# Optimization experiments

Measured on AMD Instinct MI355X. Metric: run time of the kernel, lower is better.

Reference implementation:

```python
import jax, jax.numpy as jnp
import numpy as np

B, C, H, W = 8, 64, 64, 64


def setup_inputs() -> dict:
    key = jax.random.key(0)
    ks = jax.random.split(key, 8)
    s = 1.0 / np.sqrt(C)  # keep logits in a reasonable range
    return {
        "x": jax.random.normal(ks[0], (B, C, H, W), dtype=jnp.float32),
        "Wf": jax.random.normal(ks[1], (C, C), dtype=jnp.float32) * s,
        "bf": jax.random.normal(ks[2], (C,), dtype=jnp.float32) * s,
        "Wg": jax.random.normal(ks[3], (C, C), dtype=jnp.float32) * s,
        "bg": jax.random.normal(ks[4], (C,), dtype=jnp.float32) * s,
        "Wh": jax.random.normal(ks[5], (C, C), dtype=jnp.float32) * s,
        "bh": jax.random.normal(ks[6], (C,), dtype=jnp.float32) * s,
        "gamma": jax.random.normal(ks[7], (1,), dtype=jnp.float32),
    }


def reference(x, Wf, bf, Wg, bg, Wh, bh, gamma):
    b, c, h, w = x.shape
    n = h * w
    xf = x.reshape(b, c, n)  # [B, C, N]
    # 1x1 convs == per-pixel channel GEMMs
    f = jnp.einsum("oc,bcn->bon", Wf, xf) + bf[None, :, None]  # [B, C, N]
    g = jnp.einsum("oc,bcn->bon", Wg, xf) + bg[None, :, None]
    hh = jnp.einsum("oc,bcn->bon", Wh, xf) + bh[None, :, None]
    # att_in[b, i, j] = f[b, :, i] . g[b, :, j]  (f_x permuted then bmm with g_x)
    att = jax.nn.softmax(jnp.einsum("bci,bcj->bij", f, g), axis=-1)  # [B, N, N]
    # torch.bmm(h_x, attention): out[b, c, j] = sum_i h[b, c, i] * att[b, i, j]
    out = jnp.einsum("bci,bij->bcj", hh, att).reshape(b, c, h, w)
    return gamma[0] * out + x
```

## Files before the change

### kernel.cpp

```cpp
#include <hip/hip_runtime.h>

#define BB 8
#define CC 64
#define NN 4096
#define ICH 4
#define JCH 8
#define LOG2E 1.4426950408889634f

typedef float f32x4  __attribute__((ext_vector_type(4)));
typedef float f32x16 __attribute__((ext_vector_type(16)));
typedef _Float16 half8_t __attribute__((ext_vector_type(8)));
typedef _Float16 half4_t __attribute__((ext_vector_type(4)));


__global__ __launch_bounds__(64) void qkv_kernel(
    const float* __restrict__ x,
    const float* __restrict__ Wf, const float* __restrict__ bf,
    const float* __restrict__ Wg, const float* __restrict__ bg,
    const float* __restrict__ Wh, const float* __restrict__ bh,
    _Float16* __restrict__ fT, _Float16* __restrict__ gT,
    _Float16* __restrict__ hT)
{
    const int split = blockIdx.x;
    const int z     = split >> 2;
    const int o0    = (split & 3) * 16;
    const int n     = blockIdx.y * 64 + threadIdx.x;
    const int b     = blockIdx.z;
    const float* W    = (z == 0) ? Wf : ((z == 1) ? Wg : Wh);
    const float* bias = (z == 0) ? bf : ((z == 1) ? bg : bh);

    float xv[CC];
    const float* xp = x + (size_t)b * CC * NN + n;
#pragma unroll
    for (int c = 0; c < CC; ++c) xv[c] = xp[(size_t)c * NN];

    if (z < 2) {
        _Float16* dst = ((z == 0) ? fT : gT) + (size_t)(b * NN + n) * CC + o0;
        const float scale = (z == 0) ? LOG2E : 1.0f;
#pragma unroll
        for (int o8 = 0; o8 < 2; ++o8) {
            half8_t v;
#pragma unroll
            for (int oo = 0; oo < 8; ++oo) {
                const int o = o0 + o8 * 8 + oo;
                float acc = bias[o];
#pragma unroll
                for (int c = 0; c < CC; ++c) acc += W[o * CC + c] * xv[c];
                v[oo] = (_Float16)(acc * scale);
            }
            *(half8_t*)(dst + o8 * 8) = v;
        }
    } else {
        _Float16* hdst = hT + ((size_t)(b * (NN / 32) + (n >> 5)) * CC) * 32 + (n & 31);
#pragma unroll
        for (int o = o0; o < o0 + 16; ++o) {
            float acc = bias[o];
#pragma unroll
            for (int c = 0; c < CC; ++c) acc += W[o * CC + c] * xv[c];
            hdst[o * 32] = (_Float16)acc;
        }
    }
}

__global__ __launch_bounds__(256, 4) void stats_kernel(
    const _Float16* __restrict__ fT, const _Float16* __restrict__ gT,
    float* __restrict__ lpart)
{
    __shared__ _Float16 gbuf[2][64][72];

    const int lane = threadIdx.x & 63;
    const int wv   = threadIdx.x >> 6;
    const int b    = blockIdx.y;
    const int jc   = blockIdx.z;
    const int i0   = blockIdx.x * 128 + wv * 32;
    const int l31  = lane & 31;
    const int q5   = lane >> 5;

    half8_t a[4];
    const _Float16* fa = fT + (size_t)(b * NN + i0 + l31) * CC + q5 * 8;
#pragma unroll
    for (int kc = 0; kc < 4; ++kc) a[kc] = *(const half8_t*)(fa + kc * 16);

    const _Float16* gchunk = gT + (size_t)(b * NN + jc * (NN / JCH)) * CC;
    const int T = NN / JCH / 64;

    const int srow = wv * 16 + (lane >> 3);
    const int scol = (lane & 7) * 8;

    {
        const half8_t v0 = *(const half8_t*)(gchunk + (size_t)srow * CC + scol);
        const half8_t v1 = *(const half8_t*)(gchunk + (size_t)(srow + 8) * CC + scol);
        *(half8_t*)&gbuf[0][srow][scol] = v0;
        *(half8_t*)&gbuf[0][srow + 8][scol] = v1;
    }
    __syncthreads();

    float l16[16];
#pragma unroll
    for (int r = 0; r < 16; ++r) l16[r] = 0.f;

    for (int t = 0; t < T; ++t) {
        const int buf = t & 1;
        const bool pf = (t + 1 < T);
        half8_t p0, p1;
        if (pf) {
            const _Float16* src = gchunk + (size_t)((t + 1) * 64 + srow) * CC + scol;
            p0 = *(const half8_t*)(src);
            p1 = *(const half8_t*)(src + 8 * CC);
        }
#pragma unroll
        for (int js = 0; js < 2; ++js) {
            const _Float16* grow = &gbuf[buf][js * 32 + l31][0] + q5 * 8;
            f32x16 s = {};
#pragma unroll
            for (int kc = 0; kc < 4; ++kc) {
                const half8_t bfr = *(const half8_t*)(grow + kc * 16);
                s = __builtin_amdgcn_mfma_f32_32x32x16_f16(a[kc], bfr, s, 0, 0, 0);
            }
#pragma unroll
            for (int r = 0; r < 16; ++r) l16[r] += __builtin_exp2f(s[r]);
        }
        if (pf) {
            *(half8_t*)&gbuf[buf ^ 1][srow][scol] = p0;
            *(half8_t*)&gbuf[buf ^ 1][srow + 8][scol] = p1;
        }
        __syncthreads();
    }

#pragma unroll
    for (int r = 0; r < 16; ++r) {
#pragma unroll
        for (int off = 1; off < 32; off <<= 1)
            l16[r] += __shfl_xor(l16[r], off);
    }

    if (l31 == 0) {
        float* lp = lpart + (size_t)jc * BB * NN + b * NN + i0;
#pragma unroll
        for (int rb = 0; rb < 4; ++rb) {
            f32x4 v;
#pragma unroll
            for (int k = 0; k < 4; ++k) v[k] = l16[rb * 4 + k];
            *(f32x4*)(lp + rb * 8 + q5 * 4) = v;
        }
    }
}

__global__ __launch_bounds__(256) void rmerge_kernel(
    const float* __restrict__ lpart, float* __restrict__ nbias)
{
    const int idx = blockIdx.x * 256 + threadIdx.x;
    float s = 0.f;
#pragma unroll
    for (int jc = 0; jc < JCH; ++jc) s += lpart[(size_t)jc * BB * NN + idx];
    nbias[idx] = -__builtin_log2f(s);
}

__global__ __launch_bounds__(256, 4) void attn_kernel(
    const _Float16* __restrict__ fT, const _Float16* __restrict__ gT,
    const _Float16* __restrict__ hT, const float* __restrict__ nbias,
    _Float16* __restrict__ pout)
{
    __shared__ _Float16 fbuf[2][32][72];
    __shared__ _Float16 hbuf[2][64][40];
    __shared__ _Float16 Pbuf[4][32][40];

    const int lane = threadIdx.x & 63;
    const int wv   = threadIdx.x >> 6;
    const int b    = blockIdx.y;
    const int ic   = blockIdx.z;
    const int l31  = lane & 31;
    const int q5   = lane >> 5;
    const int j0   = blockIdx.x * 128 + wv * 32;
    const int j    = j0 + l31;

    half8_t bg[4];
    const _Float16* grow = gT + (size_t)(b * NN + j) * CC + q5 * 8;
#pragma unroll
    for (int kc = 0; kc < 4; ++kc) bg[kc] = *(const half8_t*)(grow + kc * 16);

    f32x16 acc[2] = {};

    const int ibase = ic * (NN / ICH);
    const _Float16* fchunk = fT + ((size_t)b * NN + ibase) * CC;
    const _Float16* htile0 = hT + ((size_t)(b * (NN / 32) + ibase / 32) * CC) * 32;
    const float*    nb     = nbias + b * NN + ibase;
    const int T = (NN / ICH) / 32;

    const int tid    = threadIdx.x;
    const int frow_s = tid >> 3;
    const int fcol_s = (tid & 7) * 8;
    const int hoff_s = tid * 8;
    const int hrow_s = tid >> 2;
    const int hcol_s = (tid & 3) * 8;

    {
        const half8_t fv = *(const half8_t*)(fchunk + (size_t)frow_s * CC + fcol_s);
        const half8_t hv = *(const half8_t*)(htile0 + hoff_s);
        *(half8_t*)&fbuf[0][frow_s][fcol_s] = fv;
        *(half8_t*)&hbuf[0][hrow_s][hcol_s] = hv;
    }
    __syncthreads();

    for (int t = 0; t < T; ++t) {
        const int buf = t & 1;
        const bool pf = (t + 1 < T);
        half8_t pfv, phv;
        if (pf) {
            pfv = *(const half8_t*)(fchunk + (size_t)((t + 1) * 32 + frow_s) * CC + fcol_s);
            phv = *(const half8_t*)(htile0 + (size_t)(t + 1) * CC * 32 + hoff_s);
        }

        f32x16 s;
        {
#pragma unroll
            for (int rb = 0; rb < 4; ++rb) {
                const f32x4 n4 = *(const f32x4*)(nb + t * 32 + rb * 8 + q5 * 4);
#pragma unroll
                for (int k = 0; k < 4; ++k) s[rb * 4 + k] = n4[k];
            }
        }
        const _Float16* frow = &fbuf[buf][l31][0] + q5 * 8;
#pragma unroll
        for (int kc = 0; kc < 4; ++kc) {
            const half8_t af = *(const half8_t*)(frow + kc * 16);
            s = __builtin_amdgcn_mfma_f32_32x32x16_f16(af, bg[kc], s, 0, 0, 0);
        }
#pragma unroll
        for (int rb = 0; rb < 4; ++rb) {
            half4_t pv;
#pragma unroll
            for (int k = 0; k < 4; ++k)
                pv[k] = (_Float16)__builtin_exp2f(s[rb * 4 + k]);
            *(half4_t*)&Pbuf[wv][l31][rb * 8 + q5 * 4] = pv;
        }
        __builtin_amdgcn_wave_barrier();

#pragma unroll
        for (int kk = 0; kk < 2; ++kk) {
            const half8_t pb = *(const half8_t*)(&Pbuf[wv][l31][0] + kk * 16 + q5 * 8);
#pragma unroll
            for (int ct = 0; ct < 2; ++ct) {
                const half8_t ah = *(const half8_t*)(&hbuf[buf][ct * 32 + l31][0] + kk * 16 + q5 * 8);
                acc[ct] = __builtin_amdgcn_mfma_f32_32x32x16_f16(ah, pb, acc[ct], 0, 0, 0);
            }
        }
        if (pf) {
            *(half8_t*)&fbuf[buf ^ 1][frow_s][fcol_s] = pfv;
            *(half8_t*)&hbuf[buf ^ 1][hrow_s][hcol_s] = phv;
        }
        __syncthreads();
    }

    _Float16* pb_out = pout + (((size_t)ic * BB + b) * CC) * NN;
#pragma unroll
    for (int ct = 0; ct < 2; ++ct) {
#pragma unroll
        for (int r = 0; r < 16; ++r) {
            const int c = ct * 32 + (r & 3) + 8 * (r >> 2) + 4 * q5;
            pb_out[(size_t)c * NN + j] = (_Float16)acc[ct][r];
        }
    }
}

__global__ __launch_bounds__(256) void combine_kernel(
    const float* __restrict__ x, const float* __restrict__ gammap,
    const _Float16* __restrict__ pout, float* __restrict__ out)
{
    const float gam = gammap[0];
    const size_t i8 = ((size_t)blockIdx.x * 256 + threadIdx.x) * 8;
    const size_t TOT = (size_t)BB * CC * NN;

    float s[8] = {0.f, 0.f, 0.f, 0.f, 0.f, 0.f, 0.f, 0.f};
#pragma unroll
    for (int ic = 0; ic < ICH; ++ic) {
        const half8_t p = *(const half8_t*)(pout + ic * TOT + i8);
#pragma unroll
        for (int k = 0; k < 8; ++k) s[k] += (float)p[k];
    }
    const f32x4 x0 = *(const f32x4*)(x + i8);
    const f32x4 x1 = *(const f32x4*)(x + i8 + 4);
    f32x4 o0, o1;
#pragma unroll
    for (int k = 0; k < 4; ++k) { o0[k] = gam * s[k] + x0[k]; o1[k] = gam * s[k + 4] + x1[k]; }
    *(f32x4*)(out + i8) = o0;
    *(f32x4*)(out + i8 + 4) = o1;
}

extern "C" void kernel_launch(void* const* d_in, const int* in_sizes, int n_in,
                              void* d_out, int out_size, void* d_ws, size_t ws_size,
                              hipStream_t stream) {
    const float* x     = (const float*)d_in[0];
    const float* Wf    = (const float*)d_in[1];
    const float* bf    = (const float*)d_in[2];
    const float* Wg    = (const float*)d_in[3];
    const float* bg    = (const float*)d_in[4];
    const float* Wh    = (const float*)d_in[5];
    const float* bh    = (const float*)d_in[6];
    const float* gamma = (const float*)d_in[7];
    float* out = (float*)d_out;

    const size_t TOT = (size_t)BB * CC * NN;
    _Float16* fT   = (_Float16*)d_ws;
    _Float16* gT   = fT + TOT;
    _Float16* hT   = gT + TOT;
    _Float16* pout = hT + TOT;
    float* lpart   = (float*)(pout + (size_t)ICH * TOT);
    float* nbias   = lpart + (size_t)JCH * BB * NN;

    qkv_kernel<<<dim3(12, NN / 64, BB), 64, 0, stream>>>(
        x, Wf, bf, Wg, bg, Wh, bh, fT, gT, hT);
    stats_kernel<<<dim3(NN / 128, BB, JCH), 256, 0, stream>>>(fT, gT, lpart);
    rmerge_kernel<<<dim3(BB * NN / 256), 256, 0, stream>>>(lpart, nbias);
    attn_kernel<<<dim3(NN / 128, BB, ICH), 256, 0, stream>>>(fT, gT, hT, nbias, pout);
    combine_kernel<<<dim3(TOT / (256 * 8)), 256, 0, stream>>>(x, gamma, pout, out);
}
```

Before: 191.9 us.

## Keep softmax probabilities in registers via cross-lane shuffle and double i-split

The attention kernel no longer writes exp'd scores to a shared-memory P buffer and reads them back as the MFMA B operand. It rearranges the accumulator layout into operand layout with lane-xor-32 shuffles, which removes LDS traffic and a wave barrier per tile. It also doubles the number of i-chunks from 4 to 8 when the workspace is large enough, giving more blocks for occupancy. The cost is twice the partial-output traffic in the combine kernel.

```diff
diff --git a/kernel.cpp b/kernel.cpp
--- a/kernel.cpp
+++ b/kernel.cpp
@@ -3,7 +3,6 @@
 #define BB 8
 #define CC 64
 #define NN 4096
-#define ICH 4
 #define JCH 8
 #define LOG2E 1.4426950408889634f
 
@@ -11,6 +10,9 @@
 typedef float f32x16 __attribute__((ext_vector_type(16)));
 typedef _Float16 half8_t __attribute__((ext_vector_type(8)));
 typedef _Float16 half4_t __attribute__((ext_vector_type(4)));
+typedef _Float16 half2_t __attribute__((ext_vector_type(2)));
+
+typedef union { half8_t v8; half2_t v2[4]; } h8u;
 
 
 __global__ __launch_bounds__(64) void qkv_kernel(
@@ -163,16 +165,15 @@
 {
     __shared__ _Float16 fbuf[2][32][72];
     __shared__ _Float16 hbuf[2][64][40];
-    __shared__ _Float16 Pbuf[4][32][40];
 
     const int lane = threadIdx.x & 63;
     const int wv   = threadIdx.x >> 6;
     const int b    = blockIdx.y;
     const int ic   = blockIdx.z;
+    const int nic  = gridDim.z;
     const int l31  = lane & 31;
     const int q5   = lane >> 5;
-    const int j0   = blockIdx.x * 128 + wv * 32;
-    const int j    = j0 + l31;
+    const int j    = blockIdx.x * 128 + wv * 32 + l31;
 
     half8_t bg[4];
     const _Float16* grow = gT + (size_t)(b * NN + j) * CC + q5 * 8;
@@ -181,11 +182,12 @@
 
     f32x16 acc[2] = {};
 
-    const int ibase = ic * (NN / ICH);
+    const int ichunk = NN / nic;
+    const int ibase  = ic * ichunk;
     const _Float16* fchunk = fT + ((size_t)b * NN + ibase) * CC;
     const _Float16* htile0 = hT + ((size_t)(b * (NN / 32) + ibase / 32) * CC) * 32;
     const float*    nb     = nbias + b * NN + ibase;
-    const int T = (NN / ICH) / 32;
+    const int T = ichunk / 32;
 
     const int tid    = threadIdx.x;
     const int frow_s = tid >> 3;
@@ -226,25 +228,46 @@
             const half8_t af = *(const half8_t*)(frow + kc * 16);
             s = __builtin_amdgcn_mfma_f32_32x32x16_f16(af, bg[kc], s, 0, 0, 0);
         }
-#pragma unroll
-        for (int rb = 0; rb < 4; ++rb) {
-            half4_t pv;
-#pragma unroll
-            for (int k = 0; k < 4; ++k)
-                pv[k] = (_Float16)__builtin_exp2f(s[rb * 4 + k]);
-            *(half4_t*)&Pbuf[wv][l31][rb * 8 + q5 * 4] = pv;
-        }
-        __builtin_amdgcn_wave_barrier();
-
-#pragma unroll
-        for (int kk = 0; kk < 2; ++kk) {
-            const half8_t pb = *(const half8_t*)(&Pbuf[wv][l31][0] + kk * 16 + q5 * 8);
-#pragma unroll
-            for (int ct = 0; ct < 2; ++ct) {
-                const half8_t ah = *(const half8_t*)(&hbuf[buf][ct * 32 + l31][0] + kk * 16 + q5 * 8);
-                acc[ct] = __builtin_amdgcn_mfma_f32_32x32x16_f16(ah, pb, acc[ct], 0, 0, 0);
-            }
-        }
+
+        half2_t P[8];
+#pragma unroll
+        for (int r8 = 0; r8 < 8; ++r8) {
+            half2_t v;
+            v[0] = (_Float16)__builtin_exp2f(s[r8 * 2]);
+            v[1] = (_Float16)__builtin_exp2f(s[r8 * 2 + 1]);
+            P[r8] = v;
+        }
+
+        const int sA = __builtin_bit_cast(int, q5 ? P[0] : P[2]);
+        const int sB = __builtin_bit_cast(int, q5 ? P[1] : P[3]);
+        const int sC = __builtin_bit_cast(int, q5 ? P[4] : P[6]);
+        const int sD = __builtin_bit_cast(int, q5 ? P[5] : P[7]);
+        const half2_t rA = __builtin_bit_cast(half2_t, __shfl_xor(sA, 32, 64));
+        const half2_t rB = __builtin_bit_cast(half2_t, __shfl_xor(sB, 32, 64));
+        const half2_t rC = __builtin_bit_cast(half2_t, __shfl_xor(sC, 32, 64));
+        const half2_t rD = __builtin_bit_cast(half2_t, __shfl_xor(sD, 32, 64));
+
+        h8u B0, B1;
+        B0.v2[0] = q5 ? rA   : P[0];
+        B0.v2[1] = q5 ? rB   : P[1];
+        B0.v2[2] = q5 ? P[2] : rA;
+        B0.v2[3] = q5 ? P[3] : rB;
+        B1.v2[0] = q5 ? rC   : P[4];
+        B1.v2[1] = q5 ? rD   : P[5];
+        B1.v2[2] = q5 ? P[6] : rC;
+        B1.v2[3] = q5 ? P[7] : rD;
+
+#pragma unroll
+        for (int ct = 0; ct < 2; ++ct) {
+            const half8_t ah0 = *(const half8_t*)(&hbuf[buf][ct * 32 + l31][0] + q5 * 8);
+            acc[ct] = __builtin_amdgcn_mfma_f32_32x32x16_f16(ah0, B0.v8, acc[ct], 0, 0, 0);
+        }
+#pragma unroll
+        for (int ct = 0; ct < 2; ++ct) {
+            const half8_t ah1 = *(const half8_t*)(&hbuf[buf][ct * 32 + l31][0] + 16 + q5 * 8);
+            acc[ct] = __builtin_amdgcn_mfma_f32_32x32x16_f16(ah1, B1.v8, acc[ct], 0, 0, 0);
+        }
+
         if (pf) {
             *(half8_t*)&fbuf[buf ^ 1][frow_s][fcol_s] = pfv;
             *(half8_t*)&hbuf[buf ^ 1][hrow_s][hcol_s] = phv;
@@ -265,15 +288,14 @@
 
 __global__ __launch_bounds__(256) void combine_kernel(
     const float* __restrict__ x, const float* __restrict__ gammap,
-    const _Float16* __restrict__ pout, float* __restrict__ out)
+    const _Float16* __restrict__ pout, float* __restrict__ out, int nic)
 {
     const float gam = gammap[0];
     const size_t i8 = ((size_t)blockIdx.x * 256 + threadIdx.x) * 8;
     const size_t TOT = (size_t)BB * CC * NN;
 
     float s[8] = {0.f, 0.f, 0.f, 0.f, 0.f, 0.f, 0.f, 0.f};
-#pragma unroll
-    for (int ic = 0; ic < ICH; ++ic) {
+    for (int ic = 0; ic < nic; ++ic) {
         const half8_t p = *(const half8_t*)(pout + ic * TOT + i8);
 #pragma unroll
         for (int k = 0; k < 8; ++k) s[k] += (float)p[k];
@@ -301,17 +323,20 @@
     float* out = (float*)d_out;
 
     const size_t TOT = (size_t)BB * CC * NN;
+    const size_t fixed = 3 * TOT * 2 + (size_t)JCH * BB * NN * 4 + (size_t)BB * NN * 4;
+    const int nic = (ws_size >= fixed + 8 * TOT * 2) ? 8 : 4;
+
     _Float16* fT   = (_Float16*)d_ws;
     _Float16* gT   = fT + TOT;
     _Float16* hT   = gT + TOT;
     _Float16* pout = hT + TOT;
-    float* lpart   = (float*)(pout + (size_t)ICH * TOT);
+    float* lpart   = (float*)(pout + (size_t)nic * TOT);
     float* nbias   = lpart + (size_t)JCH * BB * NN;
 
     qkv_kernel<<<dim3(12, NN / 64, BB), 64, 0, stream>>>(
         x, Wf, bf, Wg, bg, Wh, bh, fT, gT, hT);
     stats_kernel<<<dim3(NN / 128, BB, JCH), 256, 0, stream>>>(fT, gT, lpart);
     rmerge_kernel<<<dim3(BB * NN / 256), 256, 0, stream>>>(lpart, nbias);
-    attn_kernel<<<dim3(NN / 128, BB, ICH), 256, 0, stream>>>(fT, gT, hT, nbias, pout);
-    combine_kernel<<<dim3(TOT / (256 * 8)), 256, 0, stream>>>(x, gamma, pout, out);
-}
+    attn_kernel<<<dim3(NN / 128, BB, nic), 256, 0, stream>>>(fT, gT, hT, nbias, pout);
+    combine_kernel<<<dim3(TOT / (256 * 8)), 256, 0, stream>>>(x, gamma, pout, out, nic);
+}
```

Result: slower. 204.0 us (+6.3%).

## Keep attention probabilities in registers via lane shuffles and widen i-tile to 64

Applied to the files above, without the earlier changes.

The attention kernel no longer writes the exponentiated scores to shared memory and reads them back. It packs them to fp16 pairs and rearranges them across the two half-waves with xor-32 shuffles, so they form the B operand of the second MFMA directly. The i-tile per iteration doubles from 32 to 64 rows, which halves the number of block barriers and double-buffer swaps per chunk. In exchange, shared memory per block grows and each thread holds more prefetch registers, which may affect occupancy.

```diff
diff --git a/kernel.cpp b/kernel.cpp
--- a/kernel.cpp
+++ b/kernel.cpp
@@ -3,14 +3,14 @@
 #define BB 8
 #define CC 64
 #define NN 4096
-#define ICH 4
+#define NIC 4
 #define JCH 8
 #define LOG2E 1.4426950408889634f
 
 typedef float f32x4  __attribute__((ext_vector_type(4)));
 typedef float f32x16 __attribute__((ext_vector_type(16)));
 typedef _Float16 half8_t __attribute__((ext_vector_type(8)));
-typedef _Float16 half4_t __attribute__((ext_vector_type(4)));
+typedef int int4v __attribute__((ext_vector_type(4)));
 
 
 __global__ __launch_bounds__(64) void qkv_kernel(
@@ -161,9 +161,8 @@
     const _Float16* __restrict__ hT, const float* __restrict__ nbias,
     _Float16* __restrict__ pout)
 {
-    __shared__ _Float16 fbuf[2][32][72];
-    __shared__ _Float16 hbuf[2][64][40];
-    __shared__ _Float16 Pbuf[4][32][40];
+    __shared__ _Float16 fbuf[2][64][72];
+    __shared__ _Float16 hbuf[2][64][72];
 
     const int lane = threadIdx.x & 63;
     const int wv   = threadIdx.x >> 6;
@@ -171,8 +170,7 @@
     const int ic   = blockIdx.z;
     const int l31  = lane & 31;
     const int q5   = lane >> 5;
-    const int j0   = blockIdx.x * 128 + wv * 32;
-    const int j    = j0 + l31;
+    const int j    = blockIdx.x * 128 + wv * 32 + l31;
 
     half8_t bg[4];
     const _Float16* grow = gT + (size_t)(b * NN + j) * CC + q5 * 8;
@@ -181,73 +179,104 @@
 
     f32x16 acc[2] = {};
 
-    const int ibase = ic * (NN / ICH);
+    const int ichunk = NN / NIC;
+    const int ibase  = ic * ichunk;
     const _Float16* fchunk = fT + ((size_t)b * NN + ibase) * CC;
-    const _Float16* htile0 = hT + ((size_t)(b * (NN / 32) + ibase / 32) * CC) * 32;
+    const _Float16* hchunk = hT + ((size_t)(b * (NN / 32) + ibase / 32) * CC) * 32;
     const float*    nb     = nbias + b * NN + ibase;
-    const int T = (NN / ICH) / 32;
+    const int T = ichunk / 64;
 
     const int tid    = threadIdx.x;
-    const int frow_s = tid >> 3;
-    const int fcol_s = (tid & 7) * 8;
-    const int hoff_s = tid * 8;
+    const int frow_s = tid >> 2;
+    const int fcol_s = (tid & 3) * 16;
     const int hrow_s = tid >> 2;
     const int hcol_s = (tid & 3) * 8;
 
     {
-        const half8_t fv = *(const half8_t*)(fchunk + (size_t)frow_s * CC + fcol_s);
-        const half8_t hv = *(const half8_t*)(htile0 + hoff_s);
-        *(half8_t*)&fbuf[0][frow_s][fcol_s] = fv;
-        *(half8_t*)&hbuf[0][hrow_s][hcol_s] = hv;
+        const half8_t f0 = *(const half8_t*)(fchunk + (size_t)frow_s * CC + fcol_s);
+        const half8_t f1 = *(const half8_t*)(fchunk + (size_t)frow_s * CC + fcol_s + 8);
+        const half8_t h0 = *(const half8_t*)(hchunk + tid * 8);
+        const half8_t h1 = *(const half8_t*)(hchunk + 2048 + tid * 8);
+        *(half8_t*)&fbuf[0][frow_s][fcol_s]     = f0;
+        *(half8_t*)&fbuf[0][frow_s][fcol_s + 8] = f1;
+        *(half8_t*)&hbuf[0][hrow_s][hcol_s]      = h0;
+        *(half8_t*)&hbuf[0][hrow_s][32 + hcol_s] = h1;
     }
     __syncthreads();
 
     for (int t = 0; t < T; ++t) {
         const int buf = t & 1;
         const bool pf = (t + 1 < T);
-        half8_t pfv, phv;
+        half8_t pf0, pf1, ph0, ph1;
         if (pf) {
-            pfv = *(const half8_t*)(fchunk + (size_t)((t + 1) * 32 + frow_s) * CC + fcol_s);
-            phv = *(const half8_t*)(htile0 + (size_t)(t + 1) * CC * 32 + hoff_s);
-        }
-
-        f32x16 s;
-        {
+            const _Float16* fsrc = fchunk + (size_t)((t + 1) * 64 + frow_s) * CC + fcol_s;
+            const _Float16* hsrc = hchunk + (size_t)(t + 1) * 4096 + tid * 8;
+            pf0 = *(const half8_t*)(fsrc);
+            pf1 = *(const half8_t*)(fsrc + 8);
+            ph0 = *(const half8_t*)(hsrc);
+            ph1 = *(const half8_t*)(hsrc + 2048);
+        }
+
+#pragma unroll
+        for (int ih = 0; ih < 2; ++ih) {
+            f32x16 s;
 #pragma unroll
             for (int rb = 0; rb < 4; ++rb) {
-                const f32x4 n4 = *(const f32x4*)(nb + t * 32 + rb * 8 + q5 * 4);
+                const f32x4 n4 = *(const f32x4*)(nb + t * 64 + ih * 32 + rb * 8 + q5 * 4);
 #pragma unroll
                 for (int k = 0; k < 4; ++k) s[rb * 4 + k] = n4[k];
             }
-        }
-        const _Float16* frow = &fbuf[buf][l31][0] + q5 * 8;
-#pragma unroll
-        for (int kc = 0; kc < 4; ++kc) {
-            const half8_t af = *(const half8_t*)(frow + kc * 16);
-            s = __builtin_amdgcn_mfma_f32_32x32x16_f16(af, bg[kc], s, 0, 0, 0);
-        }
-#pragma unroll
-        for (int rb = 0; rb < 4; ++rb) {
-            half4_t pv;
-#pragma unroll
-            for (int k = 0; k < 4; ++k)
-                pv[k] = (_Float16)__builtin_exp2f(s[rb * 4 + k]);
-            *(half4_t*)&Pbuf[wv][l31][rb * 8 + q5 * 4] = pv;
-        }
-        __builtin_amdgcn_wave_barrier();
-
-#pragma unroll
-        for (int kk = 0; kk < 2; ++kk) {
-            const half8_t pb = *(const half8_t*)(&Pbuf[wv][l31][0] + kk * 16 + q5 * 8);
+            const _Float16* frow = &fbuf[buf][ih * 32 + l31][0] + q5 * 8;
+#pragma unroll
+            for (int kc = 0; kc < 4; ++kc) {
+                const half8_t af = *(const half8_t*)(frow + kc * 16);
+                s = __builtin_amdgcn_mfma_f32_32x32x16_f16(af, bg[kc], s, 0, 0, 0);
+            }
+
+            int e[8];
+#pragma unroll
+            for (int r8 = 0; r8 < 8; ++r8) {
+                e[r8] = __builtin_bit_cast(int, __builtin_amdgcn_cvt_pkrtz(
+                    __builtin_exp2f(s[r8 * 2]), __builtin_exp2f(s[r8 * 2 + 1])));
+            }
+
+            const int sA = q5 ? e[0] : e[2];
+            const int sB = q5 ? e[1] : e[3];
+            const int sC = q5 ? e[4] : e[6];
+            const int sD = q5 ? e[5] : e[7];
+            const int rA = __shfl_xor(sA, 32, 64);
+            const int rB = __shfl_xor(sB, 32, 64);
+            const int rC = __shfl_xor(sC, 32, 64);
+            const int rD = __shfl_xor(sD, 32, 64);
+            int4v b0, b1;
+            b0[0] = q5 ? rA   : e[0];
+            b0[1] = q5 ? rB   : e[1];
+            b0[2] = q5 ? e[2] : rA;
+            b0[3] = q5 ? e[3] : rB;
+            b1[0] = q5 ? rC   : e[4];
+            b1[1] = q5 ? rD   : e[5];
+            b1[2] = q5 ? e[6] : rC;
+            b1[3] = q5 ? e[7] : rD;
+            const half8_t B0 = __builtin_bit_cast(half8_t, b0);
+            const half8_t B1 = __builtin_bit_cast(half8_t, b1);
+
 #pragma unroll
             for (int ct = 0; ct < 2; ++ct) {
-                const half8_t ah = *(const half8_t*)(&hbuf[buf][ct * 32 + l31][0] + kk * 16 + q5 * 8);
-                acc[ct] = __builtin_amdgcn_mfma_f32_32x32x16_f16(ah, pb, acc[ct], 0, 0, 0);
-            }
-        }
+                const half8_t ah0 = *(const half8_t*)(&hbuf[buf][ct * 32 + l31][0] + ih * 32 + q5 * 8);
+                acc[ct] = __builtin_amdgcn_mfma_f32_32x32x16_f16(ah0, B0, acc[ct], 0, 0, 0);
+            }
+#pragma unroll
+            for (int ct = 0; ct < 2; ++ct) {
+                const half8_t ah1 = *(const half8_t*)(&hbuf[buf][ct * 32 + l31][0] + ih * 32 + 16 + q5 * 8);
+                acc[ct] = __builtin_amdgcn_mfma_f32_32x32x16_f16(ah1, B1, acc[ct], 0, 0, 0);
+            }
+        }
+
         if (pf) {
-            *(half8_t*)&fbuf[buf ^ 1][frow_s][fcol_s] = pfv;
-            *(half8_t*)&hbuf[buf ^ 1][hrow_s][hcol_s] = phv;
+            *(half8_t*)&fbuf[buf ^ 1][frow_s][fcol_s]     = pf0;
+            *(half8_t*)&fbuf[buf ^ 1][frow_s][fcol_s + 8] = pf1;
+            *(half8_t*)&hbuf[buf ^ 1][hrow_s][hcol_s]      = ph0;
+            *(half8_t*)&hbuf[buf ^ 1][hrow_s][32 + hcol_s] = ph1;
         }
         __syncthreads();
     }
@@ -273,7 +302,7 @@
 
     float s[8] = {0.f, 0.f, 0.f, 0.f, 0.f, 0.f, 0.f, 0.f};
 #pragma unroll
-    for (int ic = 0; ic < ICH; ++ic) {
+    for (int ic = 0; ic < NIC; ++ic) {
         const half8_t p = *(const half8_t*)(pout + ic * TOT + i8);
 #pragma unroll
         for (int k = 0; k < 8; ++k) s[k] += (float)p[k];
@@ -305,13 +334,13 @@
     _Float16* gT   = fT + TOT;
     _Float16* hT   = gT + TOT;
     _Float16* pout = hT + TOT;
-    float* lpart   = (float*)(pout + (size_t)ICH * TOT);
+    float* lpart   = (float*)(pout + (size_t)NIC * TOT);
     float* nbias   = lpart + (size_t)JCH * BB * NN;
 
     qkv_kernel<<<dim3(12, NN / 64, BB), 64, 0, stream>>>(
         x, Wf, bf, Wg, bg, Wh, bh, fT, gT, hT);
     stats_kernel<<<dim3(NN / 128, BB, JCH), 256, 0, stream>>>(fT, gT, lpart);
     rmerge_kernel<<<dim3(BB * NN / 256), 256, 0, stream>>>(lpart, nbias);
-    attn_kernel<<<dim3(NN / 128, BB, ICH), 256, 0, stream>>>(fT, gT, hT, nbias, pout);
+    attn_kernel<<<dim3(NN / 128, BB, NIC), 256, 0, stream>>>(fT, gT, hT, nbias, pout);
     combine_kernel<<<dim3(TOT / (256 * 8)), 256, 0, stream>>>(x, gamma, pout, out);
 }
```

After: 200.0 us. 4.2% more time.
